# Performance work log

Measured on AMD Instinct MI355X. Metric: run time of the kernel, lower is better.

Reference implementation:

```python
import jax, jax.numpy as jnp
import numpy as np

T, D, E, I, TOP_K = 2048, 2048, 8, 2048, 2
SOFTCAP = 30.0


def setup_inputs() -> dict:
    key = jax.random.key(0)
    ks = jax.random.split(key, 5)
    s = 0.02  # realistic init scale
    return {
        "x": jax.random.normal(ks[0], (T, D), dtype=jnp.float32),
        "w_gate": jax.random.normal(ks[1], (E, D), dtype=jnp.float32) * s,
        "w1": jax.random.normal(ks[2], (E, I, D), dtype=jnp.float32) * s,
        "w3": jax.random.normal(ks[3], (E, I, D), dtype=jnp.float32) * s,
        "w2": jax.random.normal(ks[4], (E, D, I), dtype=jnp.float32) * s,
        "top_k": TOP_K,
    }


def reference(x, w_gate, w1, w3, w2, top_k):
    # Router gating linear in fp32 (ReplicatedLinear, bias=False)
    logits = jnp.einsum("td,ed->te", x.astype(jnp.float32), w_gate)  # [T,E]
    # Softcapped routing logits: cap * tanh(logits / cap)
    logits = SOFTCAP * jnp.tanh(logits / SOFTCAP)
    probs = jax.nn.softmax(logits, axis=-1)                          # [T,E]
    vals, idx = jax.lax.top_k(probs, top_k)                          # [T,k]
    num_experts = w_gate.shape[0]
    # Dense combine weights: zeros except top-k softmax probs (no renorm, Grok-1 style)
    combine = (jax.nn.one_hot(idx, num_experts, dtype=probs.dtype) * vals[..., None]).sum(axis=1)  # [T,E]
    combine = combine.astype(x.dtype)
    # Grok GLU experts: gelu(x@w1^T) * (x@w3^T) @ w2^T, evaluated per expert
    a = jnp.einsum("td,eid->tei", x, w1)  # [T,E,I]
    b = jnp.einsum("td,eid->tei", x, w3)
    h = jax.nn.gelu(a, approximate=False) * b
    y = jnp.einsum("tei,edi->ted", h, w2)  # [T,E,D]
    out = jnp.einsum("te,ted->td", combine, y)
    return out
```

## Files before the change

kernel.cpp:

```cpp
#include <hip/hip_runtime.h>
#include <hip/hip_bf16.h>
#include <math.h>

#define TT 2048
#define DD 2048
#define EE 8
#define II 2048
#define SOFTCAP 30.0f

typedef __attribute__((ext_vector_type(8))) short short8;
typedef __attribute__((ext_vector_type(4))) float f32x4;
typedef unsigned short u16;

__device__ __forceinline__ u16 f2bs(float f) {
    union { __hip_bfloat16 h; u16 u; } cv;
    cv.h = __float2bfloat16(f);
    return cv.u;
}

__device__ __forceinline__ void st_bf4(u16* p, float4 v) {
    unsigned int lo = (unsigned int)f2bs(v.x) | ((unsigned int)f2bs(v.y) << 16);
    unsigned int hi = (unsigned int)f2bs(v.z) | ((unsigned int)f2bs(v.w) << 16);
    *(uint2*)p = make_uint2(lo, hi);
}

__device__ __forceinline__ float4 ntld4(const float* p) {
    f32x4 v = __builtin_nontemporal_load((const f32x4*)p);
    return make_float4(v.x, v.y, v.z, v.w);
}
__device__ __forceinline__ void ntst4(float* p, float4 v) {
    f32x4 t = {v.x, v.y, v.z, v.w};
    __builtin_nontemporal_store(t, (f32x4*)p);
}

__device__ __forceinline__ void gload16(const void* g, void* l) {
    __builtin_amdgcn_global_load_lds(
        (const __attribute__((address_space(1))) unsigned int*)g,
        (__attribute__((address_space(3))) unsigned int*)l,
        16, 0, 0);
}

__global__ __launch_bounds__(256) void cvt3_kernel(
    const float* __restrict__ w1, const float* __restrict__ w3,
    const float* __restrict__ w2, u16* __restrict__ d1, u16* __restrict__ d3,
    u16* __restrict__ d2, long long n)
{
    const float* s;
    u16* d;
    if (blockIdx.y == 0)      { s = w2; d = d2; }
    else if (blockIdx.y == 1) { s = w1; d = d1; }
    else                      { s = w3; d = d3; }
    long long i = ((long long)blockIdx.x * 256 + threadIdx.x) * 8;
    if (i >= n) return;
    float4 a = ntld4(s + i);
    float4 b = ntld4(s + i + 4);
    st_bf4(d + i, a);
    st_bf4(d + i + 4, b);
}

__global__ __launch_bounds__(256) void router2_kernel(
    const float* __restrict__ x, const float* __restrict__ wg,
    int* __restrict__ counts, int* __restrict__ list, float* __restrict__ wlist,
    u16* __restrict__ xb)
{
    const int wid = threadIdx.x >> 6;
    const int lane = threadIdx.x & 63;
    const int t = blockIdx.x * 4 + wid;
    const float* xr = x + (size_t)t * DD;
    float acc[EE];
#pragma unroll
    for (int e = 0; e < EE; ++e) acc[e] = 0.f;
    for (int i = 0; i < DD; i += 256) {
        float4 xv = ntld4(xr + i + lane * 4);
        if (xb) st_bf4(xb + (size_t)t * DD + i + lane * 4, xv);
#pragma unroll
        for (int e = 0; e < EE; ++e) {
            float4 wv = *(const float4*)(wg + (size_t)e * DD + i + lane * 4);
            acc[e] += xv.x * wv.x + xv.y * wv.y + xv.z * wv.z + xv.w * wv.w;
        }
    }
#pragma unroll
    for (int e = 0; e < EE; ++e) {
#pragma unroll
        for (int off = 32; off > 0; off >>= 1)
            acc[e] += __shfl_xor(acc[e], off, 64);
    }
    if (lane == 0) {
        float p[EE];
        float mx = -1e30f;
#pragma unroll
        for (int e = 0; e < EE; ++e) {
            p[e] = SOFTCAP * tanhf(acc[e] / SOFTCAP);
            mx = fmaxf(mx, p[e]);
        }
        float s = 0.f;
#pragma unroll
        for (int e = 0; e < EE; ++e) { p[e] = expf(p[e] - mx); s += p[e]; }
        float inv = 1.f / s;
        int i0 = 0;
#pragma unroll
        for (int e = 1; e < EE; ++e) if (p[e] > p[i0]) i0 = e;
        int i1 = (i0 == 0) ? 1 : 0;
#pragma unroll
        for (int e = 0; e < EE; ++e) if (e != i0 && p[e] > p[i1]) i1 = e;
        int pos0 = atomicAdd(&counts[i0], 1);
        list[i0 * TT + pos0] = t * 2;
        wlist[i0 * TT + pos0] = p[i0] * inv;
        int pos1 = atomicAdd(&counts[i1], 1);
        list[i1 * TT + pos1] = t * 2 + 1;
        wlist[i1 * TT + pos1] = p[i1] * inv;
    }
}


#define SB0 __builtin_amdgcn_sched_barrier(0)

__global__ __launch_bounds__(256) void gemm_h_bf16(
    const u16* __restrict__ xb, const u16* __restrict__ w1b,
    const u16* __restrict__ w3b, const int* __restrict__ counts,
    const int* __restrict__ list, const float* __restrict__ wlist,
    u16* __restrict__ H)
{
    const int e = blockIdx.z;
    const int cnt = counts[e];
    const int m0 = blockIdx.y * 128;
    if (m0 >= cnt) return;
    const int n0 = blockIdx.x * 64;
    const int tid = threadIdx.x;
    const int lane = tid & 63;
    const int w = tid >> 6;

    __shared__ u16 As[2][128 * 32];
    __shared__ u16 W1s[2][64 * 32];
    __shared__ u16 W3s[2][64 * 32];

    const int colb = ((lane & 3) ^ ((lane >> 3) & 3)) * 8;
    const int rsub = lane >> 2;
    const int rA0 = w * 16 + rsub;
    const int rA1 = 64 + rA0;
    const int mA0 = m0 + rA0, mA1 = m0 + rA1;
    const int t0 = (mA0 < cnt) ? (list[e * TT + mA0] >> 1) : 0;
    const int t1 = (mA1 < cnt) ? (list[e * TT + mA1] >> 1) : 0;
    const u16* gA0 = xb + (size_t)t0 * DD + colb;
    const u16* gA1 = xb + (size_t)t1 * DD + colb;
    const int rW = w * 16 + rsub;
    const u16* gW1 = w1b + ((size_t)e * II + n0 + rW) * DD + colb;
    const u16* gW3 = w3b + ((size_t)e * II + n0 + rW) * DD + colb;

    const int wm = w >> 1, wn = w & 1;
    const int lr = lane & 15;
    const int quad = lane >> 4;
    const int qc = (quad ^ ((lr >> 1) & 3)) * 8;

    f32x4 accA[4][2], accB[4][2];
#pragma unroll
    for (int mi = 0; mi < 4; ++mi)
#pragma unroll
        for (int ni = 0; ni < 2; ++ni) {
            accA[mi][ni] = (f32x4)0.f;
            accB[mi][ni] = (f32x4)0.f;
        }

#define STAGE_H(u, kk) do { \
    gload16(gA0 + (kk), &As[u][(w * 16) * 32]); \
    gload16(gA1 + (kk), &As[u][(64 + w * 16) * 32]); \
    gload16(gW1 + (kk), &W1s[u][(w * 16) * 32]); \
    gload16(gW3 + (kk), &W3s[u][(w * 16) * 32]); \
} while (0)

#define HSTEP(u, j, VM, DOSTAGE) do { \
    asm volatile("s_waitcnt vmcnt(" #VM ")" ::: "memory"); \
    SB0; \
    __builtin_amdgcn_s_barrier(); \
    SB0; \
    short8 af[4], b1f[2], b3f[2]; \
    _Pragma("unroll") \
    for (int mi = 0; mi < 4; ++mi) \
        af[mi] = *(const short8*)&As[u][(wm * 64 + mi * 16 + lr) * 32 + qc]; \
    _Pragma("unroll") \
    for (int ni = 0; ni < 2; ++ni) { \
        b1f[ni] = *(const short8*)&W1s[u][(wn * 32 + ni * 16 + lr) * 32 + qc]; \
        b3f[ni] = *(const short8*)&W3s[u][(wn * 32 + ni * 16 + lr) * 32 + qc]; \
    } \
    SB0; \
    asm volatile("s_waitcnt lgkmcnt(0)" ::: "memory"); \
    SB0; \
    __builtin_amdgcn_s_barrier(); \
    SB0; \
    if (DOSTAGE) STAGE_H(u, ((j) + 2) * 32); \
    _Pragma("unroll") \
    for (int mi = 0; mi < 4; ++mi) \
        _Pragma("unroll") \
        for (int ni = 0; ni < 2; ++ni) { \
            accA[mi][ni] = __builtin_amdgcn_mfma_f32_16x16x32_bf16(af[mi], b1f[ni], accA[mi][ni], 0, 0, 0); \
            accB[mi][ni] = __builtin_amdgcn_mfma_f32_16x16x32_bf16(af[mi], b3f[ni], accB[mi][ni], 0, 0, 0); \
        } \
} while (0)

    STAGE_H(0, 0);
    STAGE_H(1, 32);

    for (int g = 0; g < 31; ++g) {
        const int j = g * 2;
        HSTEP(0, j + 0, 4, true);
        HSTEP(1, j + 1, 4, true);
    }
    HSTEP(0, 62, 4, false);
    HSTEP(1, 63, 0, false);
#undef HSTEP
#undef STAGE_H

#pragma unroll
    for (int mi = 0; mi < 4; ++mi) {
#pragma unroll
        for (int reg = 0; reg < 4; ++reg) {
            int m = m0 + wm * 64 + mi * 16 + quad * 4 + reg;
            if (m < cnt) {
                int entry = list[e * TT + m];
                float cw = wlist[e * TT + m];
                size_t hbase = (size_t)entry * II;
#pragma unroll
                for (int ni = 0; ni < 2; ++ni) {
                    int col = n0 + wn * 32 + ni * 16 + lr;
                    float a = accA[mi][ni][reg];
                    float b = accB[mi][ni][reg];
                    float g2 = 0.5f * a * (1.0f + erff(a * 0.70710678118654752f));
                    H[hbase + col] = f2bs(g2 * b * cw);
                }
            }
        }
    }
}

__global__ __launch_bounds__(256) void gemm_y_bf16(
    const u16* __restrict__ H, const u16* __restrict__ w2b,
    const int* __restrict__ counts, const int* __restrict__ list,
    float* __restrict__ Y)
{
    const int e = blockIdx.z;
    const int cnt = counts[e];
    const int m0 = blockIdx.y * 128;
    if (m0 >= cnt) return;
    const int n0 = blockIdx.x * 128;
    const int tid = threadIdx.x;
    const int lane = tid & 63;
    const int w = tid >> 6;

    __shared__ u16 As[2][128 * 32];
    __shared__ u16 Bs[2][128 * 32];

    const int colb = ((lane & 3) ^ ((lane >> 3) & 3)) * 8;
    const int rsub = lane >> 2;
    const int rA0 = w * 16 + rsub;
    const int rA1 = 64 + rA0;
    const int eA0 = (m0 + rA0 < cnt) ? list[e * TT + m0 + rA0] : 0;
    const int eA1 = (m0 + rA1 < cnt) ? list[e * TT + m0 + rA1] : 0;
    const u16* gA0 = H + (size_t)eA0 * II + colb;
    const u16* gA1 = H + (size_t)eA1 * II + colb;
    const u16* gB0 = w2b + ((size_t)e * DD + n0 + rA0) * II + colb;
    const u16* gB1 = w2b + ((size_t)e * DD + n0 + rA1) * II + colb;

    const int wm = w >> 1, wn = w & 1;
    const int lr = lane & 15;
    const int quad = lane >> 4;
    const int qc = (quad ^ ((lr >> 1) & 3)) * 8;

    f32x4 acc[4][4];
#pragma unroll
    for (int mi = 0; mi < 4; ++mi)
#pragma unroll
        for (int ni = 0; ni < 4; ++ni) acc[mi][ni] = (f32x4)0.f;

#define STAGE_Y(u, kk) do { \
    gload16(gA0 + (kk), &As[u][(w * 16) * 32]); \
    gload16(gA1 + (kk), &As[u][(64 + w * 16) * 32]); \
    gload16(gB0 + (kk), &Bs[u][(w * 16) * 32]); \
    gload16(gB1 + (kk), &Bs[u][(64 + w * 16) * 32]); \
} while (0)

#define YSTEP(u, j, VM, DOSTAGE) do { \
    asm volatile("s_waitcnt vmcnt(" #VM ")" ::: "memory"); \
    SB0; \
    __builtin_amdgcn_s_barrier(); \
    SB0; \
    short8 af[4], bf[4]; \
    _Pragma("unroll") \
    for (int mi = 0; mi < 4; ++mi) \
        af[mi] = *(const short8*)&As[u][(wm * 64 + mi * 16 + lr) * 32 + qc]; \
    _Pragma("unroll") \
    for (int ni = 0; ni < 4; ++ni) \
        bf[ni] = *(const short8*)&Bs[u][(wn * 64 + ni * 16 + lr) * 32 + qc]; \
    SB0; \
    asm volatile("s_waitcnt lgkmcnt(0)" ::: "memory"); \
    SB0; \
    __builtin_amdgcn_s_barrier(); \
    SB0; \
    if (DOSTAGE) STAGE_Y(u, ((j) + 2) * 32); \
    _Pragma("unroll") \
    for (int mi = 0; mi < 4; ++mi) \
        _Pragma("unroll") \
        for (int ni = 0; ni < 4; ++ni) \
            acc[mi][ni] = __builtin_amdgcn_mfma_f32_16x16x32_bf16(af[mi], bf[ni], acc[mi][ni], 0, 0, 0); \
} while (0)

    STAGE_Y(0, 0);
    STAGE_Y(1, 32);

    for (int g = 0; g < 31; ++g) {
        const int j = g * 2;
        YSTEP(0, j + 0, 4, true);
        YSTEP(1, j + 1, 4, true);
    }
    YSTEP(0, 62, 4, false);
    YSTEP(1, 63, 0, false);
#undef YSTEP
#undef STAGE_Y

#pragma unroll
    for (int mi = 0; mi < 4; ++mi) {
#pragma unroll
        for (int reg = 0; reg < 4; ++reg) {
            int m = m0 + wm * 64 + mi * 16 + quad * 4 + reg;
            if (m < cnt) {
                int entry = list[e * TT + m];
                float* yrow = Y + (size_t)entry * DD + n0 + wn * 64;
#pragma unroll
                for (int ni = 0; ni < 4; ++ni)
                    yrow[ni * 16 + lr] = acc[mi][ni][reg];
            }
        }
    }
}

__global__ __launch_bounds__(256) void combine_kernel(
    const float* __restrict__ Y, float* __restrict__ out)
{
    long long i4 = ((long long)blockIdx.x * 256 + threadIdx.x) * 4;
    int t = (int)(i4 >> 11);
    int d = (int)(i4 & 2047);
    float4 a = *(const float4*)(Y + (size_t)(2 * t) * DD + d);
    float4 b = *(const float4*)(Y + (size_t)(2 * t + 1) * DD + d);
    float4 r = make_float4(a.x + b.x, a.y + b.y, a.z + b.z, a.w + b.w);
    ntst4(out + i4, r);
}

__global__ __launch_bounds__(256) void gemm_h_fb(
    const float* __restrict__ x, const float* __restrict__ w1,
    const float* __restrict__ w3, const int* __restrict__ counts,
    const int* __restrict__ list, const float* __restrict__ wlist,
    __hip_bfloat16* __restrict__ H)
{
    const int e = blockIdx.z;
    const int cnt = counts[e];
    const int m0 = blockIdx.y * 128;
    if (m0 >= cnt) return;
    const int n0 = blockIdx.x * 64;
    const int tid = threadIdx.x;

    __shared__ u16 As[128][40];
    __shared__ u16 W1s[64][40];
    __shared__ u16 W3s[64][40];

    const int arow = tid >> 1;
    const int ahalf = tid & 1;
    const bool avalid = (m0 + arow) < cnt;
    const float* aptr = nullptr;
    if (avalid) {
        int entry = list[e * TT + m0 + arow];
        aptr = x + (size_t)(entry >> 1) * DD + ahalf * 16;
    }
    const int wrow = tid >> 2;
    const int wq = tid & 3;
    const float* w1ptr = w1 + ((size_t)e * II + (n0 + wrow)) * DD + wq * 8;
    const float* w3ptr = w3 + ((size_t)e * II + (n0 + wrow)) * DD + wq * 8;

    const int lane = tid & 63;
    const int wid = tid >> 6;
    const int wm = wid >> 1;
    const int wn = wid & 1;
    const int lr = lane & 15;
    const int quad = lane >> 4;

    f32x4 accA[4][2], accB[4][2];
#pragma unroll
    for (int mi = 0; mi < 4; ++mi)
#pragma unroll
        for (int ni = 0; ni < 2; ++ni) {
            accA[mi][ni] = (f32x4)0.f;
            accB[mi][ni] = (f32x4)0.f;
        }

    for (int kk = 0; kk < DD; kk += 32) {
#pragma unroll
        for (int it = 0; it < 4; ++it) {
            float4 v = make_float4(0.f, 0.f, 0.f, 0.f);
            if (avalid) v = *(const float4*)(aptr + kk + it * 4);
            st_bf4(&As[arow][ahalf * 16 + it * 4], v);
        }
#pragma unroll
        for (int it = 0; it < 2; ++it) {
            float4 v1 = *(const float4*)(w1ptr + kk + it * 4);
            st_bf4(&W1s[wrow][wq * 8 + it * 4], v1);
            float4 v3 = *(const float4*)(w3ptr + kk + it * 4);
            st_bf4(&W3s[wrow][wq * 8 + it * 4], v3);
        }
        __syncthreads();

        short8 af[4], b1f[2], b3f[2];
#pragma unroll
        for (int mi = 0; mi < 4; ++mi)
            af[mi] = *(const short8*)&As[wm * 64 + mi * 16 + lr][quad * 8];
#pragma unroll
        for (int ni = 0; ni < 2; ++ni) {
            b1f[ni] = *(const short8*)&W1s[wn * 32 + ni * 16 + lr][quad * 8];
            b3f[ni] = *(const short8*)&W3s[wn * 32 + ni * 16 + lr][quad * 8];
        }
#pragma unroll
        for (int mi = 0; mi < 4; ++mi)
#pragma unroll
            for (int ni = 0; ni < 2; ++ni) {
                accA[mi][ni] = __builtin_amdgcn_mfma_f32_16x16x32_bf16(af[mi], b1f[ni], accA[mi][ni], 0, 0, 0);
                accB[mi][ni] = __builtin_amdgcn_mfma_f32_16x16x32_bf16(af[mi], b3f[ni], accB[mi][ni], 0, 0, 0);
            }
        __syncthreads();
    }

#pragma unroll
    for (int mi = 0; mi < 4; ++mi) {
#pragma unroll
        for (int reg = 0; reg < 4; ++reg) {
            int m = m0 + wm * 64 + mi * 16 + quad * 4 + reg;
            if (m < cnt) {
                int entry = list[e * TT + m];
                float cw = wlist[e * TT + m];
                size_t hbase = (size_t)entry * II;
#pragma unroll
                for (int ni = 0; ni < 2; ++ni) {
                    int col = n0 + wn * 32 + ni * 16 + lr;
                    float a = accA[mi][ni][reg];
                    float b = accB[mi][ni][reg];
                    float g = 0.5f * a * (1.0f + erff(a * 0.70710678118654752f));
                    H[hbase + col] = __float2bfloat16(g * b * cw);
                }
            }
        }
    }
}

__global__ __launch_bounds__(256) void gemm_y_fb(
    const __hip_bfloat16* __restrict__ H, const float* __restrict__ w2,
    const int* __restrict__ counts, const int* __restrict__ list,
    float* __restrict__ out)
{
    const int e = blockIdx.z;
    const int cnt = counts[e];
    const int m0 = blockIdx.y * 128;
    if (m0 >= cnt) return;
    const int n0 = blockIdx.x * 128;
    const int tid = threadIdx.x;

    __shared__ u16 As[128][40];
    __shared__ u16 Ws[128][40];

    const int arow = tid >> 1;
    const int ahalf = tid & 1;
    const bool avalid = (m0 + arow) < cnt;
    const u16* aptr = nullptr;
    if (avalid) {
        int entry = list[e * TT + m0 + arow];
        aptr = (const u16*)H + (size_t)entry * II + ahalf * 16;
    }
    const int wrow = tid >> 1;
    const int whalf = tid & 1;
    const float* wptr = w2 + ((size_t)e * DD + (n0 + wrow)) * II + whalf * 16;

    const int lane = tid & 63;
    const int wid = tid >> 6;
    const int wm = wid >> 1;
    const int wn = wid & 1;
    const int lr = lane & 15;
    const int quad = lane >> 4;

    f32x4 acc[4][4];
#pragma unroll
    for (int mi = 0; mi < 4; ++mi)
#pragma unroll
        for (int ni = 0; ni < 4; ++ni) acc[mi][ni] = (f32x4)0.f;

    for (int kk = 0; kk < II; kk += 32) {
#pragma unroll
        for (int it = 0; it < 2; ++it) {
            int4 v = make_int4(0, 0, 0, 0);
            if (avalid) v = *(const int4*)(aptr + kk + it * 8);
            *(int4*)&As[arow][ahalf * 16 + it * 8] = v;
        }
#pragma unroll
        for (int it = 0; it < 4; ++it) {
            float4 v = *(const float4*)(wptr + kk + it * 4);
            st_bf4(&Ws[wrow][whalf * 16 + it * 4], v);
        }
        __syncthreads();

        short8 af[4], bf[4];
#pragma unroll
        for (int mi = 0; mi < 4; ++mi)
            af[mi] = *(const short8*)&As[wm * 64 + mi * 16 + lr][quad * 8];
#pragma unroll
        for (int ni = 0; ni < 4; ++ni)
            bf[ni] = *(const short8*)&Ws[wn * 64 + ni * 16 + lr][quad * 8];
#pragma unroll
        for (int mi = 0; mi < 4; ++mi)
#pragma unroll
            for (int ni = 0; ni < 4; ++ni)
                acc[mi][ni] = __builtin_amdgcn_mfma_f32_16x16x32_bf16(af[mi], bf[ni], acc[mi][ni], 0, 0, 0);
        __syncthreads();
    }

#pragma unroll
    for (int mi = 0; mi < 4; ++mi) {
#pragma unroll
        for (int reg = 0; reg < 4; ++reg) {
            int m = m0 + wm * 64 + mi * 16 + quad * 4 + reg;
            if (m < cnt) {
                int token = list[e * TT + m] >> 1;
                float* orow = out + (size_t)token * DD + n0 + wn * 64;
#pragma unroll
                for (int ni = 0; ni < 4; ++ni)
                    atomicAdd(&orow[ni * 16 + lr], acc[mi][ni][reg]);
            }
        }
    }
}

extern "C" void kernel_launch(void* const* d_in, const int* in_sizes, int n_in,
                              void* d_out, int out_size, void* d_ws, size_t ws_size,
                              hipStream_t stream) {
    const float* x  = (const float*)d_in[0];
    const float* wg = (const float*)d_in[1];
    const float* w1 = (const float*)d_in[2];
    const float* w3 = (const float*)d_in[3];
    const float* w2 = (const float*)d_in[4];
    float* out = (float*)d_out;

    char* ws = (char*)d_ws;
    int*   counts = (int*)(ws);
    int*   list   = (int*)(ws + 4096);
    float* wlist  = (float*)(ws + 4096 + 65536);
    u16*   H      = (u16*)(ws + 135168);
    const size_t NW = (size_t)EE * II * DD;
    u16*   xb  = (u16*)(ws + 135168 + 16777216);
    u16*   w1b = (u16*)((char*)xb + (size_t)TT * DD * 2);
    u16*   w3b = (u16*)((char*)w1b + NW * 2);
    u16*   w2b = (u16*)((char*)w3b + NW * 2);
    float* Y = (float*)xb;
    const size_t NEED = (size_t)135168 + 16777216 + (size_t)TT * DD * 2 + 3 * NW * 2;

    hipMemsetAsync(counts, 0, EE * sizeof(int), stream);

    if (ws_size >= NEED) {
        router2_kernel<<<TT / 4, 256, 0, stream>>>(x, wg, counts, list, wlist, xb);
        const int cvb = (int)(NW / 8 / 256);
        cvt3_kernel<<<dim3(cvb, 3), 256, 0, stream>>>(w1, w3, w2, w1b, w3b, w2b, (long long)NW);
        gemm_h_bf16<<<dim3(II / 64, TT / 128, EE), 256, 0, stream>>>(
            xb, w1b, w3b, counts, list, wlist, H);
        gemm_y_bf16<<<dim3(DD / 128, TT / 128, EE), 256, 0, stream>>>(
            H, w2b, counts, list, Y);
        combine_kernel<<<(TT * DD / 4) / 256, 256, 0, stream>>>(Y, out);
    } else {
        hipMemsetAsync(out, 0, (size_t)out_size * sizeof(float), stream);
        router2_kernel<<<TT / 4, 256, 0, stream>>>(x, wg, counts, list, wlist, nullptr);
        gemm_h_fb<<<dim3(II / 64, TT / 128, EE), 256, 0, stream>>>(
            x, w1, w3, counts, list, wlist, (__hip_bfloat16*)H);
        gemm_y_fb<<<dim3(DD / 128, TT / 128, EE), 256, 0, stream>>>(
            (const __hip_bfloat16*)H, w2, counts, list, out);
    }
}
```

Baseline: 610.3 us.

## Fuse fp32-to-bf16 weight conversion into expert GEMM loads

Removes the separate kernel that converted w1, w3 and w2 to bf16. The expert GEMMs now load fp32 weights into registers, convert them in-kernel and write them to a single-buffered LDS tile, while activations stay double-buffered via direct global-to-LDS loads. This avoids a full pass that read and wrote every weight tensor. In exchange, each weight element is re-read in fp32 by every token-tile block of its expert (twice the bytes of bf16), and the kernels take on extra register pressure, conversion ALU work and a changed barrier and waitcnt schedule.

```diff
diff --git a/kernel.cpp b/kernel.cpp
--- a/kernel.cpp
+++ b/kernel.cpp
@@ -24,6 +24,15 @@
     *(uint2*)p = make_uint2(lo, hi);
 }
 
+__device__ __forceinline__ short8 cvt8(float4 a, float4 b) {
+    short8 r;
+    r[0] = (short)f2bs(a.x); r[1] = (short)f2bs(a.y);
+    r[2] = (short)f2bs(a.z); r[3] = (short)f2bs(a.w);
+    r[4] = (short)f2bs(b.x); r[5] = (short)f2bs(b.y);
+    r[6] = (short)f2bs(b.z); r[7] = (short)f2bs(b.w);
+    return r;
+}
+
 __device__ __forceinline__ float4 ntld4(const float* p) {
     f32x4 v = __builtin_nontemporal_load((const f32x4*)p);
     return make_float4(v.x, v.y, v.z, v.w);
@@ -38,24 +47,6 @@
         (const __attribute__((address_space(1))) unsigned int*)g,
         (__attribute__((address_space(3))) unsigned int*)l,
         16, 0, 0);
-}
-
-__global__ __launch_bounds__(256) void cvt3_kernel(
-    const float* __restrict__ w1, const float* __restrict__ w3,
-    const float* __restrict__ w2, u16* __restrict__ d1, u16* __restrict__ d3,
-    u16* __restrict__ d2, long long n)
-{
-    const float* s;
-    u16* d;
-    if (blockIdx.y == 0)      { s = w2; d = d2; }
-    else if (blockIdx.y == 1) { s = w1; d = d1; }
-    else                      { s = w3; d = d3; }
-    long long i = ((long long)blockIdx.x * 256 + threadIdx.x) * 8;
-    if (i >= n) return;
-    float4 a = ntld4(s + i);
-    float4 b = ntld4(s + i + 4);
-    st_bf4(d + i, a);
-    st_bf4(d + i + 4, b);
 }
 
 __global__ __launch_bounds__(256) void router2_kernel(
@@ -116,8 +107,8 @@
 #define SB0 __builtin_amdgcn_sched_barrier(0)
 
 __global__ __launch_bounds__(256) void gemm_h_bf16(
-    const u16* __restrict__ xb, const u16* __restrict__ w1b,
-    const u16* __restrict__ w3b, const int* __restrict__ counts,
+    const u16* __restrict__ xb, const float* __restrict__ w1,
+    const float* __restrict__ w3, const int* __restrict__ counts,
     const int* __restrict__ list, const float* __restrict__ wlist,
     u16* __restrict__ H)
 {
@@ -131,8 +122,8 @@
     const int w = tid >> 6;
 
     __shared__ u16 As[2][128 * 32];
-    __shared__ u16 W1s[2][64 * 32];
-    __shared__ u16 W3s[2][64 * 32];
+    __shared__ u16 W1s[64 * 32];
+    __shared__ u16 W3s[64 * 32];
 
     const int colb = ((lane & 3) ^ ((lane >> 3) & 3)) * 8;
     const int rsub = lane >> 2;
@@ -144,14 +135,16 @@
     const u16* gA0 = xb + (size_t)t0 * DD + colb;
     const u16* gA1 = xb + (size_t)t1 * DD + colb;
     const int rW = w * 16 + rsub;
-    const u16* gW1 = w1b + ((size_t)e * II + n0 + rW) * DD + colb;
-    const u16* gW3 = w3b + ((size_t)e * II + n0 + rW) * DD + colb;
+    const float* gW1f = w1 + ((size_t)e * II + n0 + rW) * DD + colb;
+    const float* gW3f = w3 + ((size_t)e * II + n0 + rW) * DD + colb;
+    const int wslot = rW * 32 + (lane & 3) * 8;
 
     const int wm = w >> 1, wn = w & 1;
     const int lr = lane & 15;
     const int quad = lane >> 4;
     const int qc = (quad ^ ((lr >> 1) & 3)) * 8;
 
+    float4 W1r[2][2], W3r[2][2];
     f32x4 accA[4][2], accB[4][2];
 #pragma unroll
     for (int mi = 0; mi < 4; ++mi)
@@ -164,8 +157,10 @@
 #define STAGE_H(u, kk) do { \
     gload16(gA0 + (kk), &As[u][(w * 16) * 32]); \
     gload16(gA1 + (kk), &As[u][(64 + w * 16) * 32]); \
-    gload16(gW1 + (kk), &W1s[u][(w * 16) * 32]); \
-    gload16(gW3 + (kk), &W3s[u][(w * 16) * 32]); \
+    W1r[u][0] = *(const float4*)(gW1f + (kk)); \
+    W1r[u][1] = *(const float4*)(gW1f + (kk) + 4); \
+    W3r[u][0] = *(const float4*)(gW3f + (kk)); \
+    W3r[u][1] = *(const float4*)(gW3f + (kk) + 4); \
 } while (0)
 
 #define HSTEP(u, j, VM, DOSTAGE) do { \
@@ -173,21 +168,36 @@
     SB0; \
     __builtin_amdgcn_s_barrier(); \
     SB0; \
-    short8 af[4], b1f[2], b3f[2]; \
+    short8 af[4]; \
     _Pragma("unroll") \
     for (int mi = 0; mi < 4; ++mi) \
         af[mi] = *(const short8*)&As[u][(wm * 64 + mi * 16 + lr) * 32 + qc]; \
+    *(short8*)&W1s[wslot] = cvt8(W1r[u][0], W1r[u][1]); \
+    *(short8*)&W3s[wslot] = cvt8(W3r[u][0], W3r[u][1]); \
+    SB0; \
+    asm volatile("s_waitcnt lgkmcnt(0)" ::: "memory"); \
+    SB0; \
+    __builtin_amdgcn_s_barrier(); \
+    SB0; \
+    if (DOSTAGE) { \
+        gload16(gA0 + ((j) + 2) * 32, &As[u][(w * 16) * 32]); \
+        gload16(gA1 + ((j) + 2) * 32, &As[u][(64 + w * 16) * 32]); \
+    } \
+    short8 b1f[2], b3f[2]; \
     _Pragma("unroll") \
     for (int ni = 0; ni < 2; ++ni) { \
-        b1f[ni] = *(const short8*)&W1s[u][(wn * 32 + ni * 16 + lr) * 32 + qc]; \
-        b3f[ni] = *(const short8*)&W3s[u][(wn * 32 + ni * 16 + lr) * 32 + qc]; \
+        b1f[ni] = *(const short8*)&W1s[(wn * 32 + ni * 16 + lr) * 32 + qc]; \
+        b3f[ni] = *(const short8*)&W3s[(wn * 32 + ni * 16 + lr) * 32 + qc]; \
     } \
+    if (DOSTAGE) { \
+        W1r[u][0] = *(const float4*)(gW1f + ((j) + 2) * 32); \
+        W1r[u][1] = *(const float4*)(gW1f + ((j) + 2) * 32 + 4); \
+        W3r[u][0] = *(const float4*)(gW3f + ((j) + 2) * 32); \
+        W3r[u][1] = *(const float4*)(gW3f + ((j) + 2) * 32 + 4); \
+    } \
     SB0; \
     asm volatile("s_waitcnt lgkmcnt(0)" ::: "memory"); \
     SB0; \
-    __builtin_amdgcn_s_barrier(); \
-    SB0; \
-    if (DOSTAGE) STAGE_H(u, ((j) + 2) * 32); \
     _Pragma("unroll") \
     for (int mi = 0; mi < 4; ++mi) \
         _Pragma("unroll") \
@@ -202,10 +212,10 @@
 
     for (int g = 0; g < 31; ++g) {
         const int j = g * 2;
-        HSTEP(0, j + 0, 4, true);
-        HSTEP(1, j + 1, 4, true);
-    }
-    HSTEP(0, 62, 4, false);
+        HSTEP(0, j + 0, 6, true);
+        HSTEP(1, j + 1, 6, true);
+    }
+    HSTEP(0, 62, 6, false);
     HSTEP(1, 63, 0, false);
 #undef HSTEP
 #undef STAGE_H
@@ -233,7 +243,7 @@
 }
 
 __global__ __launch_bounds__(256) void gemm_y_bf16(
-    const u16* __restrict__ H, const u16* __restrict__ w2b,
+    const u16* __restrict__ H, const float* __restrict__ w2,
     const int* __restrict__ counts, const int* __restrict__ list,
     float* __restrict__ Y)
 {
@@ -247,7 +257,7 @@
     const int w = tid >> 6;
 
     __shared__ u16 As[2][128 * 32];
-    __shared__ u16 Bs[2][128 * 32];
+    __shared__ u16 Bs[128 * 32];
 
     const int colb = ((lane & 3) ^ ((lane >> 3) & 3)) * 8;
     const int rsub = lane >> 2;
@@ -257,14 +267,17 @@
     const int eA1 = (m0 + rA1 < cnt) ? list[e * TT + m0 + rA1] : 0;
     const u16* gA0 = H + (size_t)eA0 * II + colb;
     const u16* gA1 = H + (size_t)eA1 * II + colb;
-    const u16* gB0 = w2b + ((size_t)e * DD + n0 + rA0) * II + colb;
-    const u16* gB1 = w2b + ((size_t)e * DD + n0 + rA1) * II + colb;
+    const float* gB0f = w2 + ((size_t)e * DD + n0 + rA0) * II + colb;
+    const float* gB1f = w2 + ((size_t)e * DD + n0 + rA1) * II + colb;
+    const int wslot0 = rA0 * 32 + (lane & 3) * 8;
+    const int wslot1 = rA1 * 32 + (lane & 3) * 8;
 
     const int wm = w >> 1, wn = w & 1;
     const int lr = lane & 15;
     const int quad = lane >> 4;
     const int qc = (quad ^ ((lr >> 1) & 3)) * 8;
 
+    float4 B0r[2][2], B1r[2][2];
     f32x4 acc[4][4];
 #pragma unroll
     for (int mi = 0; mi < 4; ++mi)
@@ -274,8 +287,10 @@
 #define STAGE_Y(u, kk) do { \
     gload16(gA0 + (kk), &As[u][(w * 16) * 32]); \
     gload16(gA1 + (kk), &As[u][(64 + w * 16) * 32]); \
-    gload16(gB0 + (kk), &Bs[u][(w * 16) * 32]); \
-    gload16(gB1 + (kk), &Bs[u][(64 + w * 16) * 32]); \
+    B0r[u][0] = *(const float4*)(gB0f + (kk)); \
+    B0r[u][1] = *(const float4*)(gB0f + (kk) + 4); \
+    B1r[u][0] = *(const float4*)(gB1f + (kk)); \
+    B1r[u][1] = *(const float4*)(gB1f + (kk) + 4); \
 } while (0)
 
 #define YSTEP(u, j, VM, DOSTAGE) do { \
@@ -283,19 +298,34 @@
     SB0; \
     __builtin_amdgcn_s_barrier(); \
     SB0; \
-    short8 af[4], bf[4]; \
+    short8 af[4]; \
     _Pragma("unroll") \
     for (int mi = 0; mi < 4; ++mi) \
         af[mi] = *(const short8*)&As[u][(wm * 64 + mi * 16 + lr) * 32 + qc]; \
+    *(short8*)&Bs[wslot0] = cvt8(B0r[u][0], B0r[u][1]); \
+    *(short8*)&Bs[wslot1] = cvt8(B1r[u][0], B1r[u][1]); \
+    SB0; \
+    asm volatile("s_waitcnt lgkmcnt(0)" ::: "memory"); \
+    SB0; \
+    __builtin_amdgcn_s_barrier(); \
+    SB0; \
+    if (DOSTAGE) { \
+        gload16(gA0 + ((j) + 2) * 32, &As[u][(w * 16) * 32]); \
+        gload16(gA1 + ((j) + 2) * 32, &As[u][(64 + w * 16) * 32]); \
+    } \
+    short8 bf[4]; \
     _Pragma("unroll") \
     for (int ni = 0; ni < 4; ++ni) \
-        bf[ni] = *(const short8*)&Bs[u][(wn * 64 + ni * 16 + lr) * 32 + qc]; \
+        bf[ni] = *(const short8*)&Bs[(wn * 64 + ni * 16 + lr) * 32 + qc]; \
+    if (DOSTAGE) { \
+        B0r[u][0] = *(const float4*)(gB0f + ((j) + 2) * 32); \
+        B0r[u][1] = *(const float4*)(gB0f + ((j) + 2) * 32 + 4); \
+        B1r[u][0] = *(const float4*)(gB1f + ((j) + 2) * 32); \
+        B1r[u][1] = *(const float4*)(gB1f + ((j) + 2) * 32 + 4); \
+    } \
     SB0; \
     asm volatile("s_waitcnt lgkmcnt(0)" ::: "memory"); \
     SB0; \
-    __builtin_amdgcn_s_barrier(); \
-    SB0; \
-    if (DOSTAGE) STAGE_Y(u, ((j) + 2) * 32); \
     _Pragma("unroll") \
     for (int mi = 0; mi < 4; ++mi) \
         _Pragma("unroll") \
@@ -308,10 +338,10 @@
 
     for (int g = 0; g < 31; ++g) {
         const int j = g * 2;
-        YSTEP(0, j + 0, 4, true);
-        YSTEP(1, j + 1, 4, true);
-    }
-    YSTEP(0, 62, 4, false);
+        YSTEP(0, j + 0, 6, true);
+        YSTEP(1, j + 1, 6, true);
+    }
+    YSTEP(0, 62, 6, false);
     YSTEP(1, 63, 0, false);
 #undef YSTEP
 #undef STAGE_Y
@@ -547,24 +577,18 @@
     int*   list   = (int*)(ws + 4096);
     float* wlist  = (float*)(ws + 4096 + 65536);
     u16*   H      = (u16*)(ws + 135168);
-    const size_t NW = (size_t)EE * II * DD;
-    u16*   xb  = (u16*)(ws + 135168 + 16777216);
-    u16*   w1b = (u16*)((char*)xb + (size_t)TT * DD * 2);
-    u16*   w3b = (u16*)((char*)w1b + NW * 2);
-    u16*   w2b = (u16*)((char*)w3b + NW * 2);
-    float* Y = (float*)xb;
-    const size_t NEED = (size_t)135168 + 16777216 + (size_t)TT * DD * 2 + 3 * NW * 2;
+    u16*   xb     = (u16*)(ws + 135168 + 16777216);
+    float* Y      = (float*)(ws + 135168 + 16777216 + 8388608);
+    const size_t NEED = (size_t)135168 + 16777216 + 8388608 + 33554432;
 
     hipMemsetAsync(counts, 0, EE * sizeof(int), stream);
 
     if (ws_size >= NEED) {
         router2_kernel<<<TT / 4, 256, 0, stream>>>(x, wg, counts, list, wlist, xb);
-        const int cvb = (int)(NW / 8 / 256);
-        cvt3_kernel<<<dim3(cvb, 3), 256, 0, stream>>>(w1, w3, w2, w1b, w3b, w2b, (long long)NW);
         gemm_h_bf16<<<dim3(II / 64, TT / 128, EE), 256, 0, stream>>>(
-            xb, w1b, w3b, counts, list, wlist, H);
+            xb, w1, w3, counts, list, wlist, H);
         gemm_y_bf16<<<dim3(DD / 128, TT / 128, EE), 256, 0, stream>>>(
-            H, w2b, counts, list, Y);
+            H, w2, counts, list, Y);
         combine_kernel<<<(TT * DD / 4) / 256, 256, 0, stream>>>(Y, out);
     } else {
         hipMemsetAsync(out, 0, (size_t)out_size * sizeof(float), stream);
```

Result: slower. 726.3 us (+19.0%).

## Fuse router and weight conversion into one prep kernel; interleave expert block order

Applied to the files above, without the earlier changes.

Merges the weight fp32-to-bf16 conversion and the router/x-conversion into a single prep kernel launch, so the router's blocks run alongside the conversion and one launch is dropped. Both GEMM kernels remap their block indices so consecutive blocks cycle across the 8 experts rather than iterating expert-major. The remap spreads early-exit blocks (tiles past an expert's token count) and the per-expert weight traffic more evenly across CUs and caches. The fallback path keeps a separate router kernel.

```diff
diff --git a/kernel.cpp b/kernel.cpp
--- a/kernel.cpp
+++ b/kernel.cpp
@@ -40,39 +40,41 @@
         16, 0, 0);
 }
 
-__global__ __launch_bounds__(256) void cvt3_kernel(
+#define CVB ((EE * II * DD) / 8 / 256)
+
+__global__ __launch_bounds__(256) void prep_kernel(
+    const float* __restrict__ x, const float* __restrict__ wg,
     const float* __restrict__ w1, const float* __restrict__ w3,
-    const float* __restrict__ w2, u16* __restrict__ d1, u16* __restrict__ d3,
-    u16* __restrict__ d2, long long n)
+    const float* __restrict__ w2,
+    int* __restrict__ counts, int* __restrict__ list, float* __restrict__ wlist,
+    u16* __restrict__ xb, u16* __restrict__ w1b, u16* __restrict__ w3b,
+    u16* __restrict__ w2b)
 {
-    const float* s;
-    u16* d;
-    if (blockIdx.y == 0)      { s = w2; d = d2; }
-    else if (blockIdx.y == 1) { s = w1; d = d1; }
-    else                      { s = w3; d = d3; }
-    long long i = ((long long)blockIdx.x * 256 + threadIdx.x) * 8;
-    if (i >= n) return;
-    float4 a = ntld4(s + i);
-    float4 b = ntld4(s + i + 4);
-    st_bf4(d + i, a);
-    st_bf4(d + i + 4, b);
-}
-
-__global__ __launch_bounds__(256) void router2_kernel(
-    const float* __restrict__ x, const float* __restrict__ wg,
-    int* __restrict__ counts, int* __restrict__ list, float* __restrict__ wlist,
-    u16* __restrict__ xb)
-{
+    int b = blockIdx.x;
+    if (b < 3 * CVB) {
+        const float* s;
+        u16* d;
+        if (b < CVB)            { s = w2; d = w2b; }
+        else if (b < 2 * CVB)   { s = w1; d = w1b; b -= CVB; }
+        else                    { s = w3; d = w3b; b -= 2 * CVB; }
+        long long i = ((long long)b * 256 + threadIdx.x) * 8;
+        float4 a = ntld4(s + i);
+        float4 c = ntld4(s + i + 4);
+        st_bf4(d + i, a);
+        st_bf4(d + i + 4, c);
+        return;
+    }
+    const int rb = b - 3 * CVB;
     const int wid = threadIdx.x >> 6;
     const int lane = threadIdx.x & 63;
-    const int t = blockIdx.x * 4 + wid;
+    const int t = rb * 4 + wid;
     const float* xr = x + (size_t)t * DD;
     float acc[EE];
 #pragma unroll
     for (int e = 0; e < EE; ++e) acc[e] = 0.f;
     for (int i = 0; i < DD; i += 256) {
         float4 xv = ntld4(xr + i + lane * 4);
-        if (xb) st_bf4(xb + (size_t)t * DD + i + lane * 4, xv);
+        st_bf4(xb + (size_t)t * DD + i + lane * 4, xv);
 #pragma unroll
         for (int e = 0; e < EE; ++e) {
             float4 wv = *(const float4*)(wg + (size_t)e * DD + i + lane * 4);
@@ -121,11 +123,14 @@
     const int* __restrict__ list, const float* __restrict__ wlist,
     u16* __restrict__ H)
 {
-    const int e = blockIdx.z;
+    const int lin = blockIdx.x + 32 * (blockIdx.y + 16 * blockIdx.z);
+    const int e = lin & 7;
+    const int idx = (blockIdx.x >> 3) + 4 * blockIdx.y + 64 * blockIdx.z;
+    const int m0 = (idx & 15) * 128;
+    const int n0 = (idx >> 4) * 64;
+
     const int cnt = counts[e];
-    const int m0 = blockIdx.y * 128;
     if (m0 >= cnt) return;
-    const int n0 = blockIdx.x * 64;
     const int tid = threadIdx.x;
     const int lane = tid & 63;
     const int w = tid >> 6;
@@ -237,11 +242,14 @@
     const int* __restrict__ counts, const int* __restrict__ list,
     float* __restrict__ Y)
 {
-    const int e = blockIdx.z;
+    const int lin = blockIdx.x + 16 * (blockIdx.y + 16 * blockIdx.z);
+    const int e = lin & 7;
+    const int idx = (blockIdx.x >> 3) + 2 * blockIdx.y + 32 * blockIdx.z;
+    const int m0 = (idx & 15) * 128;
+    const int n0 = (idx >> 4) * 128;
+
     const int cnt = counts[e];
-    const int m0 = blockIdx.y * 128;
     if (m0 >= cnt) return;
-    const int n0 = blockIdx.x * 128;
     const int tid = threadIdx.x;
     const int lane = tid & 63;
     const int w = tid >> 6;
@@ -342,6 +350,58 @@
     float4 b = *(const float4*)(Y + (size_t)(2 * t + 1) * DD + d);
     float4 r = make_float4(a.x + b.x, a.y + b.y, a.z + b.z, a.w + b.w);
     ntst4(out + i4, r);
+}
+
+__global__ __launch_bounds__(256) void router2_kernel(
+    const float* __restrict__ x, const float* __restrict__ wg,
+    int* __restrict__ counts, int* __restrict__ list, float* __restrict__ wlist)
+{
+    const int wid = threadIdx.x >> 6;
+    const int lane = threadIdx.x & 63;
+    const int t = blockIdx.x * 4 + wid;
+    const float* xr = x + (size_t)t * DD;
+    float acc[EE];
+#pragma unroll
+    for (int e = 0; e < EE; ++e) acc[e] = 0.f;
+    for (int i = 0; i < DD; i += 256) {
+        float4 xv = *(const float4*)(xr + i + lane * 4);
+#pragma unroll
+        for (int e = 0; e < EE; ++e) {
+            float4 wv = *(const float4*)(wg + (size_t)e * DD + i + lane * 4);
+            acc[e] += xv.x * wv.x + xv.y * wv.y + xv.z * wv.z + xv.w * wv.w;
+        }
+    }
+#pragma unroll
+    for (int e = 0; e < EE; ++e) {
+#pragma unroll
+        for (int off = 32; off > 0; off >>= 1)
+            acc[e] += __shfl_xor(acc[e], off, 64);
+    }
+    if (lane == 0) {
+        float p[EE];
+        float mx = -1e30f;
+#pragma unroll
+        for (int e = 0; e < EE; ++e) {
+            p[e] = SOFTCAP * tanhf(acc[e] / SOFTCAP);
+            mx = fmaxf(mx, p[e]);
+        }
+        float s = 0.f;
+#pragma unroll
+        for (int e = 0; e < EE; ++e) { p[e] = expf(p[e] - mx); s += p[e]; }
+        float inv = 1.f / s;
+        int i0 = 0;
+#pragma unroll
+        for (int e = 1; e < EE; ++e) if (p[e] > p[i0]) i0 = e;
+        int i1 = (i0 == 0) ? 1 : 0;
+#pragma unroll
+        for (int e = 0; e < EE; ++e) if (e != i0 && p[e] > p[i1]) i1 = e;
+        int pos0 = atomicAdd(&counts[i0], 1);
+        list[i0 * TT + pos0] = t * 2;
+        wlist[i0 * TT + pos0] = p[i0] * inv;
+        int pos1 = atomicAdd(&counts[i1], 1);
+        list[i1 * TT + pos1] = t * 2 + 1;
+        wlist[i1 * TT + pos1] = p[i1] * inv;
+    }
 }
 
 __global__ __launch_bounds__(256) void gemm_h_fb(
@@ -558,9 +618,8 @@
     hipMemsetAsync(counts, 0, EE * sizeof(int), stream);
 
     if (ws_size >= NEED) {
-        router2_kernel<<<TT / 4, 256, 0, stream>>>(x, wg, counts, list, wlist, xb);
-        const int cvb = (int)(NW / 8 / 256);
-        cvt3_kernel<<<dim3(cvb, 3), 256, 0, stream>>>(w1, w3, w2, w1b, w3b, w2b, (long long)NW);
+        prep_kernel<<<3 * CVB + TT / 4, 256, 0, stream>>>(
+            x, wg, w1, w3, w2, counts, list, wlist, xb, w1b, w3b, w2b);
         gemm_h_bf16<<<dim3(II / 64, TT / 128, EE), 256, 0, stream>>>(
             xb, w1b, w3b, counts, list, wlist, H);
         gemm_y_bf16<<<dim3(DD / 128, TT / 128, EE), 256, 0, stream>>>(
@@ -568,7 +627,7 @@
         combine_kernel<<<(TT * DD / 4) / 256, 256, 0, stream>>>(Y, out);
     } else {
         hipMemsetAsync(out, 0, (size_t)out_size * sizeof(float), stream);
-        router2_kernel<<<TT / 4, 256, 0, stream>>>(x, wg, counts, list, wlist, nullptr);
+        router2_kernel<<<TT / 4, 256, 0, stream>>>(x, wg, counts, list, wlist);
         gemm_h_fb<<<dim3(II / 64, TT / 128, EE), 256, 0, stream>>>(
             x, w1, w3, counts, list, wlist, (__hip_bfloat16*)H);
         gemm_y_fb<<<dim3(DD / 128, TT / 128, EE), 256, 0, stream>>>(
```

After: 640.7 us. 1.05x slower.

## Fold w2 bf16 conversion into gemm_h launch to overlap with GEMM

Applied to the files above, without the earlier changes.

The standalone conversion kernel now handles only w1 and w3. The w2 fp32-to-bf16 conversion moves into extra blocks of the gemm_h launch (blockIdx.x >= 32), so it can overlap with the routed GEMM work and fill CUs that would otherwise sit idle on early-exit blocks. Conversion loads also switch from nontemporal to regular loads. The grid of the first GEMM grows, and the converter blocks compete with GEMM blocks for bandwidth and scheduling slots.

```diff
diff --git a/kernel.cpp b/kernel.cpp
--- a/kernel.cpp
+++ b/kernel.cpp
@@ -40,20 +40,15 @@
         16, 0, 0);
 }
 
-__global__ __launch_bounds__(256) void cvt3_kernel(
+__global__ __launch_bounds__(256) void cvt13_kernel(
     const float* __restrict__ w1, const float* __restrict__ w3,
-    const float* __restrict__ w2, u16* __restrict__ d1, u16* __restrict__ d3,
-    u16* __restrict__ d2, long long n)
-{
-    const float* s;
-    u16* d;
-    if (blockIdx.y == 0)      { s = w2; d = d2; }
-    else if (blockIdx.y == 1) { s = w1; d = d1; }
-    else                      { s = w3; d = d3; }
+    u16* __restrict__ d1, u16* __restrict__ d3)
+{
+    const float* s = blockIdx.y ? w3 : w1;
+    u16* d = blockIdx.y ? d3 : d1;
     long long i = ((long long)blockIdx.x * 256 + threadIdx.x) * 8;
-    if (i >= n) return;
-    float4 a = ntld4(s + i);
-    float4 b = ntld4(s + i + 4);
+    float4 a = *(const float4*)(s + i);
+    float4 b = *(const float4*)(s + i + 4);
     st_bf4(d + i, a);
     st_bf4(d + i + 4, b);
 }
@@ -117,10 +112,25 @@
 
 __global__ __launch_bounds__(256) void gemm_h_bf16(
     const u16* __restrict__ xb, const u16* __restrict__ w1b,
-    const u16* __restrict__ w3b, const int* __restrict__ counts,
+    const u16* __restrict__ w3b, const float* __restrict__ w2,
+    u16* __restrict__ w2b, const int* __restrict__ counts,
     const int* __restrict__ list, const float* __restrict__ wlist,
     u16* __restrict__ H)
 {
+    if (blockIdx.x >= 32) {
+        long long base = ((long long)(blockIdx.x - 32)
+                          + 16LL * (blockIdx.y + 16 * blockIdx.z)) * 16384;
+#pragma unroll
+        for (int k2 = 0; k2 < 8; ++k2) {
+            long long i = base + k2 * 2048 + threadIdx.x * 8;
+            float4 a = *(const float4*)(w2 + i);
+            float4 c4 = *(const float4*)(w2 + i + 4);
+            st_bf4(w2b + i, a);
+            st_bf4(w2b + i + 4, c4);
+        }
+        return;
+    }
+
     const int e = blockIdx.z;
     const int cnt = counts[e];
     const int m0 = blockIdx.y * 128;
@@ -559,10 +569,9 @@
 
     if (ws_size >= NEED) {
         router2_kernel<<<TT / 4, 256, 0, stream>>>(x, wg, counts, list, wlist, xb);
-        const int cvb = (int)(NW / 8 / 256);
-        cvt3_kernel<<<dim3(cvb, 3), 256, 0, stream>>>(w1, w3, w2, w1b, w3b, w2b, (long long)NW);
-        gemm_h_bf16<<<dim3(II / 64, TT / 128, EE), 256, 0, stream>>>(
-            xb, w1b, w3b, counts, list, wlist, H);
+        cvt13_kernel<<<dim3((int)(NW / 8 / 256), 2), 256, 0, stream>>>(w1, w3, w1b, w3b);
+        gemm_h_bf16<<<dim3(32 + 16, TT / 128, EE), 256, 0, stream>>>(
+            xb, w1b, w3b, w2, w2b, counts, list, wlist, H);
         gemm_y_bf16<<<dim3(DD / 128, TT / 128, EE), 256, 0, stream>>>(
             H, w2b, counts, list, Y);
         combine_kernel<<<(TT * DD / 4) / 256, 256, 0, stream>>>(Y, out);
```

Result: slower. 646.1 us (+5.9%).
